# Performance work log

Measured on AMD Instinct MI355X. Metric: run time of the kernel, lower is better.

## Reference

```python
import jax, jax.numpy as jnp
import numpy as np

H_HEADS = 4
HEAD_QK = 64   # key_dim 256 / 4 heads
HEAD_V = 128   # value_dim 512 / 4 heads


def _ln(x, w, b, eps=1e-5):
    mu = jnp.mean(x, -1, keepdims=True)
    var = jnp.mean(jnp.square(x - mu), -1, keepdims=True)
    return (x - mu) / jnp.sqrt(var + eps) * w + b


def _gn(x, w, b, groups, eps=1e-5):
    # group norm over channel groups (per-head norm of WKV output)
    B, T, C = x.shape
    xg = x.reshape(B, T, groups, C // groups)
    mu = jnp.mean(xg, -1, keepdims=True)
    var = jnp.mean(jnp.square(xg - mu), -1, keepdims=True)
    xn = ((xg - mu) / jnp.sqrt(var + eps)).reshape(B, T, C)
    return xn * w + b


def _shift(x):
    # token shift: prepend zero, drop last (nn.ZeroPad2d((0,0,1,-1)))
    return jnp.pad(x, ((0, 0), (1, 0), (0, 0)))[:, :-1]


def setup_inputs() -> dict:
    key = jax.random.key(0)
    ks = jax.random.split(key, 32)
    B, T, C = 8, 4096, 512
    KD, VD = 256, 512        # key_dim = int(512*0.5), value_dim = int(512*1)
    LR, GLR = 32, 64         # proj_low_rank_dim, gate_low_rank_dim
    FF = 1024                # intermediate_size

    def nrm(k, shp, sc=0.02):
        return jax.random.normal(k, shp, dtype=jnp.float32) * sc

    return {
        "x": jax.random.normal(ks[0], (B, T, C), dtype=jnp.float32),
        "attn_ln_w": jnp.ones((C,), jnp.float32),
        "attn_ln_b": jnp.zeros((C,), jnp.float32),
        "mu_x": jax.random.uniform(ks[1], (C,), jnp.float32),
        "W_x1": nrm(ks[2], (C, 5 * LR)),
        "W_x2": nrm(ks[3], (5, LR, C)),
        "x_bias": jax.random.uniform(ks[4], (5, C), jnp.float32),
        "W_r": nrm(ks[5], (C, KD)),
        "W_k": nrm(ks[6], (C, KD)),
        "W_v": nrm(ks[7], (C, VD)),
        "W_g": nrm(ks[8], (C, VD)),
        "W_w1": nrm(ks[9], (C, GLR)),
        "W_w2": nrm(ks[10], (GLR, KD)),
        "b_w2": jax.random.uniform(ks[11], (KD,), jnp.float32, 0.5, 2.0),
        "u": nrm(ks[12], (H_HEADS, HEAD_QK), 0.5),
        "gn_w": jnp.ones((VD,), jnp.float32),
        "gn_b": jnp.zeros((VD,), jnp.float32),
        "W_o": nrm(ks[13], (VD, C)),
        "ffn_ln_w": jnp.ones((C,), jnp.float32),
        "ffn_ln_b": jnp.zeros((C,), jnp.float32),
        "mu_k": jax.random.uniform(ks[14], (C,), jnp.float32),
        "W_key": nrm(ks[15], (C, FF)),
        "mu_r": jax.random.uniform(ks[16], (C,), jnp.float32),
        "W_rec": nrm(ks[17], (C, C)),
        "W_val": nrm(ks[18], (FF, C)),
    }


def reference(x, attn_ln_w, attn_ln_b, mu_x, W_x1, W_x2, x_bias, W_r, W_k, W_v, W_g,
              W_w1, W_w2, b_w2, u, gn_w, gn_b, W_o, ffn_ln_w, ffn_ln_b,
              mu_k, W_key, mu_r, W_rec, W_val):
    B, T, C = x.shape
    H, K = H_HEADS, HEAD_QK

    # ---------- time mixing (RWKV6 attention) ----------
    res = x
    h = _ln(x, attn_ln_w, attn_ln_b)
    delta = _shift(h) - h
    # low-rank data-dependent lerp factors for (r, w, k, v, g)
    xx = jnp.tanh((h + delta * mu_x) @ W_x1).reshape(B, T, 5, -1)   # [B,T,5,LR]
    mus = jnp.einsum('btnr,nrh->btnh', xx, W_x2) + x_bias           # [B,T,5,C]
    mr, mw, mk, mv, mg = (mus[:, :, i] for i in range(5))
    r = ((h + delta * mr) @ W_r).reshape(B, T, H, K)
    w = jnp.tanh((h + delta * mw) @ W_w1) @ W_w2 + b_w2             # decay LoRA
    w = (-jnp.exp(w)).reshape(B, T, H, K)                           # log-decay <= 0
    k = ((h + delta * mk) @ W_k).reshape(B, T, H, K)
    v = ((h + delta * mv) @ W_v).reshape(B, T, H, -1)               # [B,T,H,V]
    g = (h + delta * mg) @ W_g                                      # output gate

    # WKV6 recurrence: o_t = r_t . (S + diag(u) k_t v_t^T); S <- diag(e^{w_t}) S + k_t v_t^T
    def step(S, inp):
        rt, kt, vt, wt = inp                      # [B,H,K],[B,H,K],[B,H,V],[B,H,K]
        kv = kt[..., :, None] * vt[..., None, :]  # [B,H,K,V]
        ot = jnp.einsum('bhk,bhkv->bhv', rt, S + u[None, :, :, None] * kv)
        return jnp.exp(wt)[..., None] * S + kv, ot

    S0 = jnp.zeros((B, H, K, v.shape[-1]), x.dtype)
    seq = (r.transpose(1, 0, 2, 3), k.transpose(1, 0, 2, 3),
           v.transpose(1, 0, 2, 3), w.transpose(1, 0, 2, 3))
    _, o = jax.lax.scan(step, S0, seq)            # o: [T,B,H,V]
    o = o.transpose(1, 0, 2, 3).reshape(B, T, -1)
    o = _gn(o, gn_w, gn_b, H) * jax.nn.silu(g)
    h = res + o @ W_o

    # ---------- channel mixing (RWKV6 FFN) ----------
    res = h
    hn = _ln(h, ffn_ln_w, ffn_ln_b)
    delta = _shift(hn) - hn
    kf = jnp.square(jax.nn.relu((hn + delta * mu_k) @ W_key))
    rf = jax.nn.sigmoid((hn + delta * mu_r) @ W_rec)
    return res + rf * (kf @ W_val)
```

## Files before the change

kernel.cpp:

```cpp
#include <hip/hip_runtime.h>
#include <hip/hip_bf16.h>
#include <hip/hip_fp16.h>
#include <math.h>

#define BB 8
#define TT 4096
#define CC 512
#define BT (BB*TT)
#define KD 256
#define VD 512
#define NSUB 64
#define SUB 64

using bf16 = __hip_bfloat16;
using f16 = _Float16;
typedef __attribute__((ext_vector_type(2))) float f32x2;
typedef __attribute__((ext_vector_type(4))) float f32x4;
typedef __attribute__((ext_vector_type(8))) short s16x8;
typedef __attribute__((ext_vector_type(8))) unsigned short u16x8;
typedef const __attribute__((address_space(1))) unsigned int gu32;
typedef __attribute__((address_space(3))) unsigned int lu32;

static __device__ __forceinline__ float bf2f(bf16 x){ return __bfloat162float(x); }
static __device__ __forceinline__ bf16 f2bf(float x){ return __float2bfloat16(x); }
static __device__ __forceinline__ float bfbits(unsigned short u){
  union { unsigned int i; float f; } x; x.i = ((unsigned int)u)<<16; return x.f;
}
static __device__ __forceinline__ unsigned short f2bfbits(float f){
  union { bf16 b; unsigned short u; } x; x.b = f2bf(f); return x.u;
}
static __device__ __forceinline__ float h2f(unsigned short u){
  f16 h; __builtin_memcpy(&h,&u,2); return (float)h;
}
static __device__ __forceinline__ void gload16(const void* g, void* l){
  __builtin_amdgcn_global_load_lds((gu32*)g, (lu32*)l, 16, 0, 0);
}

#define MiB 1048576ull
static constexpr size_t OFF_H1   = 0;
static constexpr size_t OFF_XX   = 32*MiB;
static constexpr size_t OFF_DSEG = 32*MiB;
static constexpr size_t OFF_HM   = 48*MiB;
static constexpr size_t OFF_R    = 80*MiB;
static constexpr size_t OFF_K    = 96*MiB;
static constexpr size_t OFF_V    = 112*MiB;
static constexpr size_t OFF_WD   = 144*MiB;
static constexpr size_t OFF_G    = 176*MiB;
static constexpr size_t OFF_W1T  = 208*MiB;
static constexpr size_t WT_X1  = 212*MiB;
static constexpr size_t WT_R   = WT_X1  + 262144;
static constexpr size_t WT_K   = WT_R   + 262144;
static constexpr size_t WT_V   = WT_K   + 262144;
static constexpr size_t WT_G   = WT_V   + 524288;
static constexpr size_t WT_W1  = WT_G   + 524288;
static constexpr size_t WT_W2  = WT_W1  + 65536;
static constexpr size_t WT_O   = WT_W2  + 32768;
static constexpr size_t WT_KEY = WT_O   + 524288;
static constexpr size_t WT_REC = WT_KEY + 1048576;
static constexpr size_t WT_VAL = WT_REC + 524288;
static constexpr size_t WT_X2T = WT_VAL + 1048576;
static constexpr size_t WS_NEED = WT_X2T + 163840;

__global__ __launch_bounds__(256) void wconv_t2(const float* s0, const float* s1, const float* s2,
        const float* s3, const float* s4, const float* s5, const float* s6, const float* s7,
        const float* s8, const float* s9, const float* s10, char* ws){
  struct E{int K,N,Npad; size_t off;};
  const E tab[11] = {
    {512,160,256,WT_X1},{512,256,256,WT_R},{512,256,256,WT_K},{512,512,512,WT_V},
    {512,512,512,WT_G},{512,64,64,WT_W1},{64,256,256,WT_W2},{512,512,512,WT_O},
    {512,1024,1024,WT_KEY},{512,512,512,WT_REC},{1024,512,512,WT_VAL}};
  const float* srcs[11] = {s0,s1,s2,s3,s4,s5,s6,s7,s8,s9,s10};
  int blk = blockIdx.x, i = 0, acc = 0;
  #pragma unroll 1
  for (; i<11; i++){ int nt = (tab[i].K>>6)*(tab[i].Npad>>6); if (blk < acc+nt) break; acc += nt; }
  int local = blk - acc;
  int K = tab[i].K, N = tab[i].N;
  int ntn = tab[i].Npad>>6;
  int k0 = (local/ntn)*64, n0 = (local%ntn)*64;
  const float* src = srcs[i];
  bf16* dst = (bf16*)(ws + tab[i].off);
  __shared__ float T[64][65];
  int t = threadIdx.x;
  #pragma unroll
  for (int e=0;e<16;e++){
    int idx = t + e*256; int r = idx>>6, c = idx&63;
    int n = n0 + c;
    T[r][c] = (n < N) ? src[(size_t)(k0+r)*N + n] : 0.f;
  }
  __syncthreads();
  #pragma unroll
  for (int e=0;e<16;e++){
    int idx = t + e*256; int r = idx>>6, c = idx&63;
    dst[(size_t)(n0+r)*K + k0 + c] = f2bf(T[c][r]);
  }
}

__global__ void wconv_x2(const float* __restrict__ src, bf16* __restrict__ dst){
  int idx = blockIdx.x*256 + threadIdx.x;
  int i = idx >> 14;
  int rem = idx & 16383;
  int c = rem >> 5, r = rem & 31;
  dst[idx] = f2bf(src[((size_t)i*32 + r)*512 + c]);
}

__global__ __launch_bounds__(256) void ln_bf16(const float* __restrict__ x, const float* __restrict__ w,
                                               const float* __restrict__ b, bf16* __restrict__ out){
  int bt = blockIdx.x;
  const float* row = x + (size_t)bt*CC;
  int t = threadIdx.x;
  float a0 = row[t], a1 = row[t+256];
  float s = a0 + a1, ss = a0*a0 + a1*a1;
  for (int off=32; off; off>>=1){ s += __shfl_down(s, off, 64); ss += __shfl_down(ss, off, 64); }
  __shared__ float ps[4], pss[4];
  int wv = t>>6, ln = t&63;
  if (ln==0){ ps[wv]=s; pss[wv]=ss; }
  __syncthreads();
  if (t==0){
    float S=ps[0]+ps[1]+ps[2]+ps[3], SS=pss[0]+pss[1]+pss[2]+pss[3];
    float mu = S/CC; float var = SS/CC - mu*mu;
    ps[0]=mu; pss[0]=rsqrtf(var+1e-5f);
  }
  __syncthreads();
  float mu = ps[0], inv = pss[0];
  out[(size_t)bt*CC + t]     = f2bf((a0-mu)*inv*w[t]+b[t]);
  out[(size_t)bt*CC + t+256] = f2bf((a1-mu)*inv*w[t+256]+b[t+256]);
}

__global__ void build_xm(const bf16* __restrict__ h, const float* __restrict__ mu_x, bf16* __restrict__ xm){
  size_t base = ((size_t)blockIdx.x*256 + threadIdx.x)*8;
  int c = (int)(base & (CC-1));
  size_t bt = base >> 9;
  u16x8 hv8 = *(const u16x8*)&((const unsigned short*)h)[base];
  u16x8 hp8;
  if (bt & (TT-1)) hp8 = *(const u16x8*)&((const unsigned short*)h)[base - CC];
  else { hp8 = u16x8{0,0,0,0,0,0,0,0}; }
  float m8[8];
  *(float4*)&m8[0] = *(const float4*)&mu_x[c];
  *(float4*)&m8[4] = *(const float4*)&mu_x[c+4];
  u16x8 o8;
  #pragma unroll
  for (int e=0;e<8;e++){
    float f = bfbits(hv8[e]), p = bfbits(hp8[e]);
    o8[e] = f2bfbits(f + (p-f)*m8[e]);
  }
  *(u16x8*)&((unsigned short*)xm)[base] = o8;
}

__global__ __launch_bounds__(256) void hm5_mfma(const bf16* __restrict__ h, const bf16* __restrict__ xx,
      const bf16* __restrict__ wx2t, const float* __restrict__ x_bias,
      bf16* __restrict__ hm0, bf16* __restrict__ hm1, bf16* __restrict__ hm2,
      bf16* __restrict__ hm3, bf16* __restrict__ hm4){
  __shared__ bf16 xxl[128][168];
  int bt0 = blockIdx.x*128;
  int c0 = blockIdx.y*128;
  int tid = threadIdx.x;
  #pragma unroll
  for (int p=0;p<10;p++){
    int idx = p*256 + tid;
    int row = idx/20, q = idx - row*20;
    *(uint4*)&xxl[row][q*8] = *(const uint4*)&xx[((size_t)(bt0+row))*256 + q*8];
  }
  __syncthreads();
  int wv = tid>>6, ln = tid&63;
  int wr = wv>>1, wc = wv&1;
  int ks = (ln>>4)*8;
  int l15 = ln&15;
  bf16* const outs[5] = {hm0,hm1,hm2,hm3,hm4};
  #pragma unroll
  for (int i=0;i<5;i++){
    s16x8 bq[4];
    #pragma unroll
    for (int ni=0;ni<4;ni++)
      bq[ni] = *(const s16x8*)&xxl[wc*64 + ni*16 + l15][i*32 + ks];
    f32x4 acc[4][4];
    #pragma unroll
    for (int mi=0;mi<4;mi++){
      int chb = c0 + wr*64 + mi*16 + (ln>>4)*4;
      float4 bia = *(const float4*)&x_bias[i*CC + chb];
      #pragma unroll
      for (int ni=0;ni<4;ni++){ f32x4 a = {bia.x,bia.y,bia.z,bia.w}; acc[mi][ni] = a; }
    }
    #pragma unroll
    for (int mi=0;mi<4;mi++){
      s16x8 aw = *(const s16x8*)&wx2t[((size_t)i*512 + c0 + wr*64 + mi*16 + l15)*32 + ks];
      #pragma unroll
      for (int ni=0;ni<4;ni++)
        acc[mi][ni] = __builtin_amdgcn_mfma_f32_16x16x32_bf16(aw, bq[ni], acc[mi][ni], 0,0,0);
    }
    bf16* o = outs[i];
    #pragma unroll
    for (int mi=0;mi<4;mi++){
      int ch = c0 + wr*64 + mi*16 + (ln>>4)*4;
      #pragma unroll
      for (int ni=0;ni<4;ni++){
        int tok = bt0 + wc*64 + ni*16 + l15;
        size_t base = (size_t)tok*CC + ch;
        ushort4 hv4 = *(const ushort4*)&((const unsigned short*)h)[base];
        ushort4 hp4;
        if (tok & (TT-1)) hp4 = *(const ushort4*)&((const unsigned short*)h)[base - CC];
        else { hp4.x=0; hp4.y=0; hp4.z=0; hp4.w=0; }
        ushort4 o4;
        float hv, hp, mus;
        hv = bfbits(hv4.x); hp = bfbits(hp4.x); mus = acc[mi][ni][0]; o4.x = f2bfbits(hv + (hp-hv)*mus);
        hv = bfbits(hv4.y); hp = bfbits(hp4.y); mus = acc[mi][ni][1]; o4.y = f2bfbits(hv + (hp-hv)*mus);
        hv = bfbits(hv4.z); hp = bfbits(hp4.z); mus = acc[mi][ni][2]; o4.z = f2bfbits(hv + (hp-hv)*mus);
        hv = bfbits(hv4.w); hp = bfbits(hp4.w); mus = acc[mi][ni][3]; o4.w = f2bfbits(hv + (hp-hv)*mus);
        *(ushort4*)&((unsigned short*)o)[base] = o4;
      }
    }
  }
}

enum {EP_BF16, EP_TANH_BF16, EP_NEGEXP_F16, EP_RES_F32, EP_RELU2_BF16, EP_SIG_BF16, EP_FINAL_F32};

template<int MODE>
__global__ __launch_bounds__(256) void gemm128(
    const bf16* __restrict__ A, const bf16* __restrict__ Bt, void* __restrict__ Out,
    int N, int K, const float* __restrict__ auxf, const bf16* __restrict__ auxb)
{
  __shared__ bf16 Al[128][32];
  __shared__ bf16 Bl[128][32];
  int tid = threadIdx.x;
  int nbk = N>>7;
  int q8 = gridDim.x>>3;
  int o = (blockIdx.x & 7)*q8 + (blockIdx.x>>3);
  int nb = o % nbk, mb = o / nbk;
  int m0 = mb*128, n0 = nb*128;
  int wv = tid>>6, ln = tid&63;
  int wr = wv>>1, wc = wv&1;
  f32x4 acc[4][4];
  #pragma unroll
  for (int i=0;i<4;i++) for (int j=0;j<4;j++){ f32x4 z={0.f,0.f,0.f,0.f}; acc[i][j]=z; }
  int r0 = tid>>2, k0 = (tid&3)*8;
  const int nkt = K>>5;
  for (int kt=0; kt<nkt; kt++){
    const bf16* ga = A  + (size_t)(m0+r0)*K + kt*32 + k0;
    const bf16* gb = Bt + (size_t)(n0+r0)*K + kt*32 + k0;
    gload16(ga,                 (char*)&Al[0][0] + tid*16);
    gload16(ga + (size_t)64*K,  (char*)&Al[0][0] + (tid+256)*16);
    gload16(gb,                 (char*)&Bl[0][0] + tid*16);
    gload16(gb + (size_t)64*K,  (char*)&Bl[0][0] + (tid+256)*16);
    __syncthreads();
    int ks = (ln>>4)*8;
    s16x8 af[4], bq[4];
    #pragma unroll
    for (int i=0;i<4;i++){
      af[i] = *(const s16x8*)&Al[wr*64 + i*16 + (ln&15)][ks];
      bq[i] = *(const s16x8*)&Bl[wc*64 + i*16 + (ln&15)][ks];
    }
    #pragma unroll
    for (int mi=0;mi<4;mi++)
      #pragma unroll
      for (int ni=0;ni<4;ni++)
        acc[mi][ni] = __builtin_amdgcn_mfma_f32_16x16x32_bf16(af[mi], bq[ni], acc[mi][ni], 0,0,0);
    __syncthreads();
  }
  #pragma unroll
  for (int mi=0;mi<4;mi++)
    #pragma unroll
    for (int ni=0;ni<4;ni++){
      int col = n0 + wc*64 + ni*16 + (ln&15);
      int rb  = m0 + wr*64 + mi*16 + (ln>>4)*4;
      #pragma unroll
      for (int j=0;j<4;j++){
        size_t idx = (size_t)(rb+j)*N + col;
        float val = acc[mi][ni][j];
        if constexpr(MODE==EP_BF16)           ((bf16*)Out)[idx] = f2bf(val);
        else if constexpr(MODE==EP_TANH_BF16) ((bf16*)Out)[idx] = f2bf(tanhf(val));
        else if constexpr(MODE==EP_RES_F32)   ((float*)Out)[idx] = auxf[idx] + val;
        else if constexpr(MODE==EP_RELU2_BF16){ float m = fmaxf(val,0.f); ((bf16*)Out)[idx] = f2bf(m*m); }
        else if constexpr(MODE==EP_SIG_BF16)  ((bf16*)Out)[idx] = f2bf(1.f/(1.f+expf(-val)));
        else if constexpr(MODE==EP_FINAL_F32) ((float*)Out)[idx] = auxf[idx] + bf2f(auxb[idx])*val;
      }
    }
}

template<int MODE>
__global__ __launch_bounds__(256) void gemm_bf16(
    const bf16* __restrict__ A, const bf16* __restrict__ Bt, void* __restrict__ Out,
    int N, int K, const float* __restrict__ bias)
{
  __shared__ bf16 Al[128][40];
  __shared__ bf16 Bl[64][40];
  int tid = threadIdx.x;
  int m0 = blockIdx.x*128, n0 = blockIdx.y*64;
  int wv = tid>>6, ln = tid&63;
  f32x4 acc[2][4];
  #pragma unroll
  for(int f=0;f<2;f++) for(int c=0;c<4;c++){ f32x4 z = {0.f,0.f,0.f,0.f}; acc[f][c]=z; }
  const int nkt = K>>5;
  for (int kt=0; kt<nkt; kt++){
    __syncthreads();
    {
      int c0 = tid, c1 = tid+256;
      int r = c0>>2, ko=(c0&3)*8;
      *(uint4*)&Al[r][ko] = *(const uint4*)&A[(size_t)(m0+r)*K + kt*32 + ko];
      r = c1>>2; ko=(c1&3)*8;
      *(uint4*)&Al[r][ko] = *(const uint4*)&A[(size_t)(m0+r)*K + kt*32 + ko];
      r = tid>>2; ko=(tid&3)*8;
      *(uint4*)&Bl[r][ko] = *(const uint4*)&Bt[(size_t)(n0+r)*K + kt*32 + ko];
    }
    __syncthreads();
    int ks = (ln>>4)*8;
    s16x8 af0 = *(const s16x8*)&Al[wv*32 + (ln&15)][ks];
    s16x8 af1 = *(const s16x8*)&Al[wv*32 + 16 + (ln&15)][ks];
    #pragma unroll
    for (int c=0;c<4;c++){
      s16x8 bfr = *(const s16x8*)&Bl[c*16 + (ln&15)][ks];
      acc[0][c] = __builtin_amdgcn_mfma_f32_16x16x32_bf16(af0, bfr, acc[0][c], 0,0,0);
      acc[1][c] = __builtin_amdgcn_mfma_f32_16x16x32_bf16(af1, bfr, acc[1][c], 0,0,0);
    }
  }
  #pragma unroll
  for (int f=0; f<2; f++) for (int c=0;c<4;c++){
    int col = n0 + c*16 + (ln&15);
    int rbase = m0 + wv*32 + f*16 + (ln>>4)*4;
    #pragma unroll
    for (int j=0;j<4;j++){
      size_t idx = (size_t)(rbase+j)*N + col;
      float val = acc[f][c][j];
      if constexpr(MODE==EP_TANH_BF16)      ((bf16*)Out)[idx] = f2bf(tanhf(val));
      else if constexpr(MODE==EP_NEGEXP_F16){
        float w = fmaxf(-expf(val + bias[col]), -20.f);
        ((f16*)Out)[idx] = (f16)expf(w);
      }
    }
  }
}

__global__ __launch_bounds__(128,3) void wkv_p1(const bf16* __restrict__ kbuf, const bf16* __restrict__ vbuf,
      const f16* __restrict__ ewb, bf16* __restrict__ Mseg, float* __restrict__ Dseg){
  int bhs = blockIdx.x; int bh = bhs>>6, sub = bhs&63;
  int b = bh>>2, h = bh&3;
  int tid = threadIdx.x, wv = tid>>6, ln = tid&63;
  __shared__ float vtile[16][132];
  int t0 = sub*SUB;
  size_t kqbase = ((size_t)b*TT + t0)*KD + h*64 + ln;
  float dacc = 1.f;
  f32x2 S2[32];
  #pragma unroll
  for (int p=0;p<32;p++){ f32x2 z={0.f,0.f}; S2[p]=z; }
  float wnxt = (float)ewb[kqbase];
  unsigned short qnxt = ((const unsigned short*)kbuf)[kqbase];
  #pragma unroll 1
  for (int tile=0; tile<4; tile++){
    int tb = t0 + tile*16;
    __syncthreads();
    {
      int t = tid>>3, c = (tid&7)*16;
      const unsigned short* vg = (const unsigned short*)vbuf + ((size_t)b*TT + tb + t)*VD + h*128 + c;
      u16x8 a8 = *(const u16x8*)vg;
      u16x8 b8 = *(const u16x8*)(vg+8);
      #pragma unroll
      for (int e=0;e<8;e++){ vtile[t][c+e] = bfbits(a8[e]); vtile[t][c+8+e] = bfbits(b8[e]); }
    }
    __syncthreads();
    #pragma unroll 1
    for (int tt=0;tt<16;tt++){
      int lt = tile*16+tt;
      float e = wnxt; unsigned short qcur = qnxt;
      if (lt < SUB-1){
        size_t gi = kqbase + (size_t)(lt+1)*KD;
        wnxt = (float)ewb[gi]; qnxt = ((const unsigned short*)kbuf)[gi];
      }
      dacc *= e;
      float qv = bfbits(qcur);
      f32x2 e2 = {e,e}, q2 = {qv,qv};
      #pragma unroll
      for (int vg=0;vg<16;vg++){
        f32x4 vvv = *(const f32x4*)&vtile[tt][wv*64 + vg*4];
        f32x2 vA = {vvv[0], vvv[1]}, vB = {vvv[2], vvv[3]};
        S2[vg*2]   = e2*S2[vg*2]   + q2*vA;
        S2[vg*2+1] = e2*S2[vg*2+1] + q2*vB;
      }
    }
  }
  unsigned short* M = (unsigned short*)Mseg + (size_t)bhs*8192 + (size_t)ln*128 + wv*64;
  #pragma unroll
  for (int vg=0; vg<16; vg++){
    ushort4 s4;
    s4.x = f2bfbits(S2[vg*2][0]);   s4.y = f2bfbits(S2[vg*2][1]);
    s4.z = f2bfbits(S2[vg*2+1][0]); s4.w = f2bfbits(S2[vg*2+1][1]);
    *(ushort4*)&M[vg*4] = s4;
  }
  if (wv==0) Dseg[(size_t)bhs*64 + ln] = dacc;
}

__global__ __launch_bounds__(256) void wkv_p2(bf16* __restrict__ MS, const float* __restrict__ Dseg){
  int idx = blockIdx.x*256 + threadIdx.x;
  int bh = idx>>13; int k = (idx>>7)&63; int v = idx&127;
  bf16* p = MS + (size_t)bh*NSUB*8192 + k*128 + v;
  const float* d = Dseg + (size_t)bh*NSUB*64 + k;
  float S = 0.f;
  float m = bf2f(p[0]); float D = d[0];
  #pragma unroll 1
  for (int seg=0; seg<NSUB; seg++){
    float mN=0.f, DN=0.f;
    if (seg < NSUB-1){ mN = bf2f(p[(size_t)(seg+1)*8192]); DN = d[(seg+1)*64]; }
    p[(size_t)seg*8192] = f2bf(S);
    S = D*S + m;
    m = mN; D = DN;
  }
}

__global__ __launch_bounds__(128,3) void wkv_p3(const bf16* __restrict__ rbuf, const bf16* __restrict__ kbuf,
     const bf16* __restrict__ vbuf, const f16* __restrict__ ewb, const bf16* __restrict__ Sstart,
     const float* __restrict__ uu, const bf16* __restrict__ gg,
     const float* __restrict__ gn_w, const float* __restrict__ gn_b, bf16* __restrict__ gated){
  int bhs = blockIdx.x; int bh = bhs>>6, sub = bhs&63;
  int b = bh>>2, h = bh&3;
  int tid = threadIdx.x;
  __shared__ float ew[8][68], qk[8][68], rr[8][68], bu[8];
  __shared__ unsigned short vtb[8][128];
  __shared__ float ot[8][132];
  int tq = tid>>4, cq4 = (tid&15)*4, cq8 = (tid&15)*8;
  float4 u4 = *(const float4*)&uu[h*64 + cq4];
  f32x2 S2[32];
  const unsigned short* Sst = (const unsigned short*)Sstart + (size_t)bhs*8192;
  #pragma unroll
  for (int p=0;p<32;p++){
    f32x2 s = { bfbits(Sst[(2*p)*128 + tid]), bfbits(Sst[(2*p+1)*128 + tid]) };
    S2[p] = s;
  }
  int t0 = sub*SUB;
  #pragma unroll 1
  for (int tile=0; tile<8; tile++){
    int tb = t0 + tile*8;
    {
      size_t gi = ((size_t)b*TT + tb + tq)*KD + h*64 + cq4;
      ushort4 e4s = *(const ushort4*)&((const unsigned short*)ewb)[gi];
      ew[tq][cq4+0]=h2f(e4s.x); ew[tq][cq4+1]=h2f(e4s.y); ew[tq][cq4+2]=h2f(e4s.z); ew[tq][cq4+3]=h2f(e4s.w);
      ushort4 k4 = *(const ushort4*)&((const unsigned short*)kbuf)[gi];
      ushort4 r4 = *(const ushort4*)&((const unsigned short*)rbuf)[gi];
      float q0=bfbits(k4.x),q1=bfbits(k4.y),q2=bfbits(k4.z),q3=bfbits(k4.w);
      float rv0=bfbits(r4.x),rv1=bfbits(r4.y),rv2=bfbits(r4.z),rv3=bfbits(r4.w);
      qk[tq][cq4+0]=q0; qk[tq][cq4+1]=q1; qk[tq][cq4+2]=q2; qk[tq][cq4+3]=q3;
      rr[tq][cq4+0]=rv0; rr[tq][cq4+1]=rv1; rr[tq][cq4+2]=rv2; rr[tq][cq4+3]=rv3;
      float part = rv0*q0*u4.x + rv1*q1*u4.y + rv2*q2*u4.z + rv3*q3*u4.w;
      part += __shfl_xor(part,1,64); part += __shfl_xor(part,2,64);
      part += __shfl_xor(part,4,64); part += __shfl_xor(part,8,64);
      if ((tid&15)==0) bu[tq] = part;
      *(u16x8*)&vtb[tq][cq8] = *(const u16x8*)&((const unsigned short*)vbuf)[((size_t)b*TT + tb + tq)*VD + h*128 + cq8];
    }
    __syncthreads();
    #pragma unroll 1
    for (int t=0;t<8;t++){
      float vl = bfbits(vtb[t][tid]);
      f32x2 vl2 = {vl, vl};
      f32x2 o2 = {0.f, 0.f};
      #pragma unroll
      for (int g=0;g<16;g++){
        f32x4 e4 = *(const f32x4*)&ew[t][g*4];
        f32x4 q4 = *(const f32x4*)&qk[t][g*4];
        f32x4 r4 = *(const f32x4*)&rr[t][g*4];
        f32x2 eA = {e4[0],e4[1]}, eB = {e4[2],e4[3]};
        f32x2 qA = {q4[0],q4[1]}, qB = {q4[2],q4[3]};
        f32x2 rA = {r4[0],r4[1]}, rB = {r4[2],r4[3]};
        int p = g*2;
        o2 += rA*S2[p];   S2[p]   = eA*S2[p]   + qA*vl2;
        o2 += rB*S2[p+1]; S2[p+1] = eB*S2[p+1] + qB*vl2;
      }
      float o = o2[0] + o2[1] + bu[t]*vl;
      ot[t][tid] = o;
    }
    __syncthreads();
    {
      float gw[8], gb[8];
      *(float4*)&gw[0] = *(const float4*)&gn_w[h*128+cq8];
      *(float4*)&gw[4] = *(const float4*)&gn_w[h*128+cq8+4];
      *(float4*)&gb[0] = *(const float4*)&gn_b[h*128+cq8];
      *(float4*)&gb[4] = *(const float4*)&gn_b[h*128+cq8+4];
      float o8[8];
      *(float4*)&o8[0] = *(const float4*)&ot[tq][cq8];
      *(float4*)&o8[4] = *(const float4*)&ot[tq][cq8+4];
      float s = 0.f, ss = 0.f;
      #pragma unroll
      for (int e=0;e<8;e++){ s += o8[e]; ss += o8[e]*o8[e]; }
      s += __shfl_xor(s,1,64); ss += __shfl_xor(ss,1,64);
      s += __shfl_xor(s,2,64); ss += __shfl_xor(ss,2,64);
      s += __shfl_xor(s,4,64); ss += __shfl_xor(ss,4,64);
      s += __shfl_xor(s,8,64); ss += __shfl_xor(ss,8,64);
      float mu = s*(1.f/128.f);
      float inv = rsqrtf(fmaxf(ss*(1.f/128.f) - mu*mu, 0.f) + 1e-5f);
      size_t go = ((size_t)b*TT + tb + tq)*VD + h*128 + cq8;
      u16x8 g8 = *(const u16x8*)&((const unsigned short*)gg)[go];
      u16x8 out8;
      #pragma unroll
      for (int e=0;e<8;e++){
        float xv = (o8[e]-mu)*inv*gw[e] + gb[e];
        float ga = bfbits(g8[e]);
        xv *= ga/(1.f+expf(-ga));
        out8[e] = f2bfbits(xv);
      }
      *(u16x8*)&((unsigned short*)gated)[go] = out8;
    }
    __syncthreads();
  }
}

__global__ void build_ffn_in(const bf16* __restrict__ hn, const float* __restrict__ mu_k,
                             const float* __restrict__ mu_r, bf16* __restrict__ kin, bf16* __restrict__ rin){
  size_t base = ((size_t)blockIdx.x*256 + threadIdx.x)*8;
  int c = (int)(base & (CC-1));
  size_t bt = base >> 9;
  u16x8 hv8 = *(const u16x8*)&((const unsigned short*)hn)[base];
  u16x8 hp8;
  if (bt & (TT-1)) hp8 = *(const u16x8*)&((const unsigned short*)hn)[base - CC];
  else { hp8 = u16x8{0,0,0,0,0,0,0,0}; }
  float mk8[8], mr8[8];
  *(float4*)&mk8[0] = *(const float4*)&mu_k[c];
  *(float4*)&mk8[4] = *(const float4*)&mu_k[c+4];
  *(float4*)&mr8[0] = *(const float4*)&mu_r[c];
  *(float4*)&mr8[4] = *(const float4*)&mu_r[c+4];
  u16x8 k8, r8;
  #pragma unroll
  for (int e=0;e<8;e++){
    float f = bfbits(hv8[e]), p = bfbits(hp8[e]);
    float d = p - f;
    k8[e] = f2bfbits(f + d*mk8[e]);
    r8[e] = f2bfbits(f + d*mr8[e]);
  }
  *(u16x8*)&((unsigned short*)kin)[base] = k8;
  *(u16x8*)&((unsigned short*)rin)[base] = r8;
}

extern "C" void kernel_launch(void* const* d_in, const int* in_sizes, int n_in,
                              void* d_out, int out_size, void* d_ws, size_t ws_size,
                              hipStream_t stream){
  (void)in_sizes; (void)n_in; (void)out_size;
  if (ws_size < WS_NEED) return;
  const float* x      = (const float*)d_in[0];
  const float* ln1w   = (const float*)d_in[1];
  const float* ln1b   = (const float*)d_in[2];
  const float* mu_x   = (const float*)d_in[3];
  const float* W_x1   = (const float*)d_in[4];
  const float* W_x2   = (const float*)d_in[5];
  const float* x_bias = (const float*)d_in[6];
  const float* W_r    = (const float*)d_in[7];
  const float* W_k    = (const float*)d_in[8];
  const float* W_v    = (const float*)d_in[9];
  const float* W_g    = (const float*)d_in[10];
  const float* W_w1   = (const float*)d_in[11];
  const float* W_w2   = (const float*)d_in[12];
  const float* b_w2   = (const float*)d_in[13];
  const float* u      = (const float*)d_in[14];
  const float* gn_w   = (const float*)d_in[15];
  const float* gn_b   = (const float*)d_in[16];
  const float* W_o    = (const float*)d_in[17];
  const float* ln2w   = (const float*)d_in[18];
  const float* ln2b   = (const float*)d_in[19];
  const float* mu_k   = (const float*)d_in[20];
  const float* W_key  = (const float*)d_in[21];
  const float* mu_r   = (const float*)d_in[22];
  const float* W_rec  = (const float*)d_in[23];
  const float* W_val  = (const float*)d_in[24];
  char* ws = (char*)d_ws;
  auto F  = [&](size_t off){ return (float*)(ws+off); };
  auto Bf = [&](size_t off){ return (bf16*)(ws+off); };
  float* h2 = (float*)d_out;
  bf16* Mseg = (bf16*)d_out;

  wconv_t2<<<620,256,0,stream>>>(W_x1,W_r,W_k,W_v,W_g,W_w1,W_w2,W_o,W_key,W_rec,W_val, ws);
  wconv_x2<<<320,256,0,stream>>>(W_x2, Bf(WT_X2T));

  ln_bf16<<<BT,256,0,stream>>>(x, ln1w, ln1b, Bf(OFF_H1));
  build_xm<<<BT*CC/8/256,256,0,stream>>>(Bf(OFF_H1), mu_x, Bf(OFF_HM));
  gemm128<EP_TANH_BF16><<<512,256,0,stream>>>(Bf(OFF_HM), Bf(WT_X1), Bf(OFF_XX), 256,512, nullptr,nullptr);

  bf16* hm1 = (bf16*)d_out;
  bf16* hm2 = (bf16*)((char*)d_out + 32*MiB);
  hm5_mfma<<<dim3(BT/128,4),256,0,stream>>>(Bf(OFF_H1), Bf(OFF_XX), Bf(WT_X2T), x_bias,
                                            Bf(OFF_HM), hm1, hm2, Bf(OFF_G), Bf(OFF_WD));
  gemm128<EP_BF16><<<512,256,0,stream>>>(Bf(OFF_HM), Bf(WT_R), Bf(OFF_R), 256,512, nullptr,nullptr);
  gemm_bf16<EP_TANH_BF16><<<dim3(BT/128,1),256,0,stream>>>(hm1, Bf(WT_W1), Bf(OFF_W1T), 64,512, nullptr);
  gemm128<EP_BF16><<<512,256,0,stream>>>(hm2, Bf(WT_K), Bf(OFF_K), 256,512, nullptr,nullptr);
  gemm128<EP_BF16><<<1024,256,0,stream>>>(Bf(OFF_G), Bf(WT_V), Bf(OFF_V), 512,512, nullptr,nullptr);
  gemm128<EP_BF16><<<1024,256,0,stream>>>(Bf(OFF_WD), Bf(WT_G), Bf(OFF_G), 512,512, nullptr,nullptr);
  gemm_bf16<EP_NEGEXP_F16><<<dim3(BT/128,4),256,0,stream>>>(Bf(OFF_W1T), Bf(WT_W2), (void*)F(OFF_WD), 256,64, b_w2);

  wkv_p1<<<BB*4*NSUB,128,0,stream>>>(Bf(OFF_K), Bf(OFF_V), (const f16*)F(OFF_WD), Mseg, F(OFF_DSEG));
  wkv_p2<<<BB*4*8192/256,256,0,stream>>>(Mseg, F(OFF_DSEG));
  wkv_p3<<<BB*4*NSUB,128,0,stream>>>(Bf(OFF_R), Bf(OFF_K), Bf(OFF_V), (const f16*)F(OFF_WD), Mseg, u,
                                     Bf(OFF_G), gn_w, gn_b, Bf(OFF_H1));

  gemm128<EP_RES_F32><<<1024,256,0,stream>>>(Bf(OFF_H1), Bf(WT_O), h2, 512,512, x,nullptr);

  ln_bf16<<<BT,256,0,stream>>>(h2, ln2w, ln2b, Bf(OFF_HM));
  build_ffn_in<<<BT*CC/8/256,256,0,stream>>>(Bf(OFF_HM), mu_k, mu_r, Bf(OFF_R), Bf(OFF_V));
  gemm128<EP_RELU2_BF16><<<2048,256,0,stream>>>(Bf(OFF_R), Bf(WT_KEY), Bf(OFF_WD), 1024,512, nullptr,nullptr);
  gemm128<EP_SIG_BF16><<<1024,256,0,stream>>>(Bf(OFF_V), Bf(WT_REC), Bf(OFF_H1), 512,512, nullptr,nullptr);
  gemm128<EP_FINAL_F32><<<1024,256,0,stream>>>(Bf(OFF_WD), Bf(WT_VAL), h2, 512,1024, h2, Bf(OFF_H1));
}
```

Baseline: 846.4 us.

## Batch independent projection GEMMs into grouped multi-GEMM launches

Adds a grouped GEMM kernel that takes a table of up to four independent GEMMs (K=512) and maps one flattened grid of 128x128 tiles across them, with an XCD-aware block remap. The four R/K/V/G projections and the two FFN key/receptance GEMMs now run as one launch each instead of separate launches. This cuts launch overhead and fills the tails between small GEMMs. The G output moves to a scratch buffer in d_out so it does not alias the WD input, and Mseg is relocated to compensate. The cost is a runtime mode branch in the epilogue and no double buffering in the shared load loop.

New measurement: 874.8 us. 1.03x slower.

```diff
diff --git a/kernel.cpp b/kernel.cpp
--- a/kernel.cpp
+++ b/kernel.cpp
@@ -271,6 +271,73 @@
         else if constexpr(MODE==EP_RELU2_BF16){ float m = fmaxf(val,0.f); ((bf16*)Out)[idx] = f2bf(m*m); }
         else if constexpr(MODE==EP_SIG_BF16)  ((bf16*)Out)[idx] = f2bf(1.f/(1.f+expf(-val)));
         else if constexpr(MODE==EP_FINAL_F32) ((float*)Out)[idx] = auxf[idx] + bf2f(auxb[idx])*val;
+      }
+    }
+}
+
+struct GEnt { const bf16* A; const bf16* Bt; bf16* Out; int N; int mode; int nblk; };
+struct GTab { GEnt e[4]; };
+
+__global__ __launch_bounds__(256) void gemm_multi(GTab tab, int total){
+  __shared__ bf16 Al[128][32];
+  __shared__ bf16 Bl[128][32];
+  int tid = threadIdx.x;
+  int q8 = total>>3;
+  int o = (blockIdx.x & 7)*q8 + (blockIdx.x>>3);
+  int i = 0, acc0 = 0;
+  #pragma unroll 1
+  for (; i<4; i++){ int nb = tab.e[i].nblk; if (o < acc0+nb) break; acc0 += nb; }
+  const bf16* A  = tab.e[i].A;
+  const bf16* Bt = tab.e[i].Bt;
+  bf16* Out = tab.e[i].Out;
+  int N = tab.e[i].N, mode = tab.e[i].mode;
+  int lo = o - acc0;
+  int nbk = N>>7;
+  int nb = lo % nbk, mb = lo / nbk;
+  int m0 = mb*128, n0 = nb*128;
+  int wv = tid>>6, ln = tid&63;
+  int wr = wv>>1, wc = wv&1;
+  f32x4 acc[4][4];
+  #pragma unroll
+  for (int a=0;a<4;a++) for (int b=0;b<4;b++){ f32x4 z={0.f,0.f,0.f,0.f}; acc[a][b]=z; }
+  int r0 = tid>>2, k0 = (tid&3)*8;
+  for (int kt=0; kt<16; kt++){
+    const bf16* ga = A  + (size_t)(m0+r0)*512 + kt*32 + k0;
+    const bf16* gb = Bt + (size_t)(n0+r0)*512 + kt*32 + k0;
+    gload16(ga,               (char*)&Al[0][0] + tid*16);
+    gload16(ga + (size_t)64*512, (char*)&Al[0][0] + (tid+256)*16);
+    gload16(gb,               (char*)&Bl[0][0] + tid*16);
+    gload16(gb + (size_t)64*512, (char*)&Bl[0][0] + (tid+256)*16);
+    __syncthreads();
+    int ks = (ln>>4)*8;
+    s16x8 af[4], bq[4];
+    #pragma unroll
+    for (int a=0;a<4;a++){
+      af[a] = *(const s16x8*)&Al[wr*64 + a*16 + (ln&15)][ks];
+      bq[a] = *(const s16x8*)&Bl[wc*64 + a*16 + (ln&15)][ks];
+    }
+    #pragma unroll
+    for (int mi=0;mi<4;mi++)
+      #pragma unroll
+      for (int ni=0;ni<4;ni++)
+        acc[mi][ni] = __builtin_amdgcn_mfma_f32_16x16x32_bf16(af[mi], bq[ni], acc[mi][ni], 0,0,0);
+    __syncthreads();
+  }
+  #pragma unroll
+  for (int mi=0;mi<4;mi++)
+    #pragma unroll
+    for (int ni=0;ni<4;ni++){
+      int col = n0 + wc*64 + ni*16 + (ln&15);
+      int rb  = m0 + wr*64 + mi*16 + (ln>>4)*4;
+      #pragma unroll
+      for (int j=0;j<4;j++){
+        size_t idx = (size_t)(rb+j)*N + col;
+        float val = acc[mi][ni][j];
+        float r;
+        if (mode == 0) r = val;
+        else if (mode == 1){ float m = fmaxf(val,0.f); r = m*m; }
+        else r = 1.f/(1.f+expf(-val));
+        Out[idx] = f2bf(r);
       }
     }
 }
@@ -558,7 +625,10 @@
   auto F  = [&](size_t off){ return (float*)(ws+off); };
   auto Bf = [&](size_t off){ return (bf16*)(ws+off); };
   float* h2 = (float*)d_out;
-  bf16* Mseg = (bf16*)d_out;
+  bf16* hm1 = (bf16*)d_out;
+  bf16* hm2 = (bf16*)((char*)d_out + 32*MiB);
+  bf16* gbuf = (bf16*)d_out;
+  bf16* Mseg = (bf16*)((char*)d_out + 32*MiB);
 
   wconv_t2<<<620,256,0,stream>>>(W_x1,W_r,W_k,W_v,W_g,W_w1,W_w2,W_o,W_key,W_rec,W_val, ws);
   wconv_x2<<<320,256,0,stream>>>(W_x2, Bf(WT_X2T));
@@ -567,27 +637,35 @@
   build_xm<<<BT*CC/8/256,256,0,stream>>>(Bf(OFF_H1), mu_x, Bf(OFF_HM));
   gemm128<EP_TANH_BF16><<<512,256,0,stream>>>(Bf(OFF_HM), Bf(WT_X1), Bf(OFF_XX), 256,512, nullptr,nullptr);
 
-  bf16* hm1 = (bf16*)d_out;
-  bf16* hm2 = (bf16*)((char*)d_out + 32*MiB);
   hm5_mfma<<<dim3(BT/128,4),256,0,stream>>>(Bf(OFF_H1), Bf(OFF_XX), Bf(WT_X2T), x_bias,
                                             Bf(OFF_HM), hm1, hm2, Bf(OFF_G), Bf(OFF_WD));
-  gemm128<EP_BF16><<<512,256,0,stream>>>(Bf(OFF_HM), Bf(WT_R), Bf(OFF_R), 256,512, nullptr,nullptr);
   gemm_bf16<EP_TANH_BF16><<<dim3(BT/128,1),256,0,stream>>>(hm1, Bf(WT_W1), Bf(OFF_W1T), 64,512, nullptr);
-  gemm128<EP_BF16><<<512,256,0,stream>>>(hm2, Bf(WT_K), Bf(OFF_K), 256,512, nullptr,nullptr);
-  gemm128<EP_BF16><<<1024,256,0,stream>>>(Bf(OFF_G), Bf(WT_V), Bf(OFF_V), 512,512, nullptr,nullptr);
-  gemm128<EP_BF16><<<1024,256,0,stream>>>(Bf(OFF_WD), Bf(WT_G), Bf(OFF_G), 512,512, nullptr,nullptr);
+  {
+    GTab t;
+    t.e[0] = {Bf(OFF_HM), Bf(WT_R), Bf(OFF_R), 256, 0, 512};
+    t.e[1] = {hm2,        Bf(WT_K), Bf(OFF_K), 256, 0, 512};
+    t.e[2] = {Bf(OFF_G),  Bf(WT_V), Bf(OFF_V), 512, 0, 1024};
+    t.e[3] = {Bf(OFF_WD), Bf(WT_G), gbuf,      512, 0, 1024};
+    gemm_multi<<<3072,256,0,stream>>>(t, 3072);
+  }
   gemm_bf16<EP_NEGEXP_F16><<<dim3(BT/128,4),256,0,stream>>>(Bf(OFF_W1T), Bf(WT_W2), (void*)F(OFF_WD), 256,64, b_w2);
 
   wkv_p1<<<BB*4*NSUB,128,0,stream>>>(Bf(OFF_K), Bf(OFF_V), (const f16*)F(OFF_WD), Mseg, F(OFF_DSEG));
   wkv_p2<<<BB*4*8192/256,256,0,stream>>>(Mseg, F(OFF_DSEG));
   wkv_p3<<<BB*4*NSUB,128,0,stream>>>(Bf(OFF_R), Bf(OFF_K), Bf(OFF_V), (const f16*)F(OFF_WD), Mseg, u,
-                                     Bf(OFF_G), gn_w, gn_b, Bf(OFF_H1));
+                                     gbuf, gn_w, gn_b, Bf(OFF_H1));
 
   gemm128<EP_RES_F32><<<1024,256,0,stream>>>(Bf(OFF_H1), Bf(WT_O), h2, 512,512, x,nullptr);
 
   ln_bf16<<<BT,256,0,stream>>>(h2, ln2w, ln2b, Bf(OFF_HM));
   build_ffn_in<<<BT*CC/8/256,256,0,stream>>>(Bf(OFF_HM), mu_k, mu_r, Bf(OFF_R), Bf(OFF_V));
-  gemm128<EP_RELU2_BF16><<<2048,256,0,stream>>>(Bf(OFF_R), Bf(WT_KEY), Bf(OFF_WD), 1024,512, nullptr,nullptr);
-  gemm128<EP_SIG_BF16><<<1024,256,0,stream>>>(Bf(OFF_V), Bf(WT_REC), Bf(OFF_H1), 512,512, nullptr,nullptr);
+  {
+    GTab t;
+    t.e[0] = {Bf(OFF_R), Bf(WT_KEY), Bf(OFF_WD), 1024, 1, 2048};
+    t.e[1] = {Bf(OFF_V), Bf(WT_REC), Bf(OFF_H1),  512, 2, 1024};
+    t.e[2] = {nullptr, nullptr, nullptr, 128, 0, 0};
+    t.e[3] = {nullptr, nullptr, nullptr, 128, 0, 0};
+    gemm_multi<<<3072,256,0,stream>>>(t, 3072);
+  }
   gemm128<EP_FINAL_F32><<<1024,256,0,stream>>>(Bf(OFF_WD), Bf(WT_VAL), h2, 512,1024, h2, Bf(OFF_H1));
 }
```

## Double WKV chunk kernels to 256 threads, splitting state across more lanes

Applied to the files above, without the earlier changes.

Both WKV chunk kernels (p1 state accumulation and p3 output pass) move from 128 to 256 threads per block. Each thread now holds half as much recurrent state, 32 floats instead of 64. In p1 the value dimension is split into quarters. In p3 the key dimension is split across two thread halves, whose partial outputs are summed through shared memory before the group norm. The aim is to raise occupancy and latency hiding on the sequential inner loop, at the cost of more shared-memory traffic, an extra reduction, and redundant per-thread loads of the shared decay and key scalars.

Measured after the change: 834.0 us. Within noise of the previous version (-1.5%).

```diff
diff --git a/kernel.cpp b/kernel.cpp
--- a/kernel.cpp
+++ b/kernel.cpp
@@ -328,18 +328,18 @@
   }
 }
 
-__global__ __launch_bounds__(128,3) void wkv_p1(const bf16* __restrict__ kbuf, const bf16* __restrict__ vbuf,
+__global__ __launch_bounds__(256) void wkv_p1(const bf16* __restrict__ kbuf, const bf16* __restrict__ vbuf,
       const f16* __restrict__ ewb, bf16* __restrict__ Mseg, float* __restrict__ Dseg){
   int bhs = blockIdx.x; int bh = bhs>>6, sub = bhs&63;
   int b = bh>>2, h = bh&3;
-  int tid = threadIdx.x, wv = tid>>6, ln = tid&63;
+  int tid = threadIdx.x, ln = tid&63, vq = tid>>6;
   __shared__ float vtile[16][132];
   int t0 = sub*SUB;
   size_t kqbase = ((size_t)b*TT + t0)*KD + h*64 + ln;
   float dacc = 1.f;
-  f32x2 S2[32];
-  #pragma unroll
-  for (int p=0;p<32;p++){ f32x2 z={0.f,0.f}; S2[p]=z; }
+  f32x2 S2[16];
+  #pragma unroll
+  for (int p=0;p<16;p++){ f32x2 z={0.f,0.f}; S2[p]=z; }
   float wnxt = (float)ewb[kqbase];
   unsigned short qnxt = ((const unsigned short*)kbuf)[kqbase];
   #pragma unroll 1
@@ -347,12 +347,13 @@
     int tb = t0 + tile*16;
     __syncthreads();
     {
-      int t = tid>>3, c = (tid&7)*16;
-      const unsigned short* vg = (const unsigned short*)vbuf + ((size_t)b*TT + tb + t)*VD + h*128 + c;
-      u16x8 a8 = *(const u16x8*)vg;
-      u16x8 b8 = *(const u16x8*)(vg+8);
-      #pragma unroll
-      for (int e=0;e<8;e++){ vtile[t][c+e] = bfbits(a8[e]); vtile[t][c+8+e] = bfbits(b8[e]); }
+      int t = tid>>4, c = (tid&15)*8;
+      u16x8 a8 = *(const u16x8*)&((const unsigned short*)vbuf)[((size_t)b*TT + tb + t)*VD + h*128 + c];
+      float4 lo, hi;
+      lo.x=bfbits(a8[0]); lo.y=bfbits(a8[1]); lo.z=bfbits(a8[2]); lo.w=bfbits(a8[3]);
+      hi.x=bfbits(a8[4]); hi.y=bfbits(a8[5]); hi.z=bfbits(a8[6]); hi.w=bfbits(a8[7]);
+      *(float4*)&vtile[t][c]   = lo;
+      *(float4*)&vtile[t][c+4] = hi;
     }
     __syncthreads();
     #pragma unroll 1
@@ -367,23 +368,23 @@
       float qv = bfbits(qcur);
       f32x2 e2 = {e,e}, q2 = {qv,qv};
       #pragma unroll
-      for (int vg=0;vg<16;vg++){
-        f32x4 vvv = *(const f32x4*)&vtile[tt][wv*64 + vg*4];
+      for (int vg=0;vg<8;vg++){
+        f32x4 vvv = *(const f32x4*)&vtile[tt][vq*32 + vg*4];
         f32x2 vA = {vvv[0], vvv[1]}, vB = {vvv[2], vvv[3]};
         S2[vg*2]   = e2*S2[vg*2]   + q2*vA;
         S2[vg*2+1] = e2*S2[vg*2+1] + q2*vB;
       }
     }
   }
-  unsigned short* M = (unsigned short*)Mseg + (size_t)bhs*8192 + (size_t)ln*128 + wv*64;
-  #pragma unroll
-  for (int vg=0; vg<16; vg++){
+  unsigned short* M = (unsigned short*)Mseg + (size_t)bhs*8192 + (size_t)ln*128 + vq*32;
+  #pragma unroll
+  for (int vg=0; vg<8; vg++){
     ushort4 s4;
     s4.x = f2bfbits(S2[vg*2][0]);   s4.y = f2bfbits(S2[vg*2][1]);
     s4.z = f2bfbits(S2[vg*2+1][0]); s4.w = f2bfbits(S2[vg*2+1][1]);
     *(ushort4*)&M[vg*4] = s4;
   }
-  if (wv==0) Dseg[(size_t)bhs*64 + ln] = dacc;
+  if (vq==0) Dseg[(size_t)bhs*64 + ln] = dacc;
 }
 
 __global__ __launch_bounds__(256) void wkv_p2(bf16* __restrict__ MS, const float* __restrict__ Dseg){
@@ -403,7 +404,7 @@
   }
 }
 
-__global__ __launch_bounds__(128,3) void wkv_p3(const bf16* __restrict__ rbuf, const bf16* __restrict__ kbuf,
+__global__ __launch_bounds__(256) void wkv_p3(const bf16* __restrict__ rbuf, const bf16* __restrict__ kbuf,
      const bf16* __restrict__ vbuf, const f16* __restrict__ ewb, const bf16* __restrict__ Sstart,
      const float* __restrict__ uu, const bf16* __restrict__ gg,
      const float* __restrict__ gn_w, const float* __restrict__ gn_b, bf16* __restrict__ gated){
@@ -412,14 +413,15 @@
   int tid = threadIdx.x;
   __shared__ float ew[8][68], qk[8][68], rr[8][68], bu[8];
   __shared__ unsigned short vtb[8][128];
-  __shared__ float ot[8][132];
-  int tq = tid>>4, cq4 = (tid&15)*4, cq8 = (tid&15)*8;
-  float4 u4 = *(const float4*)&uu[h*64 + cq4];
-  f32x2 S2[32];
+  __shared__ float otp[2][8][132];
+  int v = tid&127, kw = tid>>7, kbase = kw*32;
+  int tq = tid>>5, c2 = (tid&31)*2, cq4 = (tid&31)*4;
+  float2 u2 = *(const float2*)&uu[h*64 + c2];
+  f32x2 S2[16];
   const unsigned short* Sst = (const unsigned short*)Sstart + (size_t)bhs*8192;
   #pragma unroll
-  for (int p=0;p<32;p++){
-    f32x2 s = { bfbits(Sst[(2*p)*128 + tid]), bfbits(Sst[(2*p+1)*128 + tid]) };
+  for (int p=0;p<16;p++){
+    f32x2 s = { bfbits(Sst[(kbase+2*p)*128 + v]), bfbits(Sst[(kbase+2*p+1)*128 + v]) };
     S2[p] = s;
   }
   int t0 = sub*SUB;
@@ -427,32 +429,33 @@
   for (int tile=0; tile<8; tile++){
     int tb = t0 + tile*8;
     {
-      size_t gi = ((size_t)b*TT + tb + tq)*KD + h*64 + cq4;
-      ushort4 e4s = *(const ushort4*)&((const unsigned short*)ewb)[gi];
-      ew[tq][cq4+0]=h2f(e4s.x); ew[tq][cq4+1]=h2f(e4s.y); ew[tq][cq4+2]=h2f(e4s.z); ew[tq][cq4+3]=h2f(e4s.w);
-      ushort4 k4 = *(const ushort4*)&((const unsigned short*)kbuf)[gi];
-      ushort4 r4 = *(const ushort4*)&((const unsigned short*)rbuf)[gi];
-      float q0=bfbits(k4.x),q1=bfbits(k4.y),q2=bfbits(k4.z),q3=bfbits(k4.w);
-      float rv0=bfbits(r4.x),rv1=bfbits(r4.y),rv2=bfbits(r4.z),rv3=bfbits(r4.w);
-      qk[tq][cq4+0]=q0; qk[tq][cq4+1]=q1; qk[tq][cq4+2]=q2; qk[tq][cq4+3]=q3;
-      rr[tq][cq4+0]=rv0; rr[tq][cq4+1]=rv1; rr[tq][cq4+2]=rv2; rr[tq][cq4+3]=rv3;
-      float part = rv0*q0*u4.x + rv1*q1*u4.y + rv2*q2*u4.z + rv3*q3*u4.w;
+      size_t gi = ((size_t)b*TT + tb + tq)*KD + h*64 + c2;
+      ushort2 e2s = *(const ushort2*)&((const unsigned short*)ewb)[gi];
+      ew[tq][c2] = h2f(e2s.x); ew[tq][c2+1] = h2f(e2s.y);
+      ushort2 k2 = *(const ushort2*)&((const unsigned short*)kbuf)[gi];
+      ushort2 r2 = *(const ushort2*)&((const unsigned short*)rbuf)[gi];
+      float q0=bfbits(k2.x), q1=bfbits(k2.y);
+      float rv0=bfbits(r2.x), rv1=bfbits(r2.y);
+      qk[tq][c2]=q0; qk[tq][c2+1]=q1;
+      rr[tq][c2]=rv0; rr[tq][c2+1]=rv1;
+      float part = rv0*q0*u2.x + rv1*q1*u2.y;
       part += __shfl_xor(part,1,64); part += __shfl_xor(part,2,64);
       part += __shfl_xor(part,4,64); part += __shfl_xor(part,8,64);
-      if ((tid&15)==0) bu[tq] = part;
-      *(u16x8*)&vtb[tq][cq8] = *(const u16x8*)&((const unsigned short*)vbuf)[((size_t)b*TT + tb + tq)*VD + h*128 + cq8];
+      part += __shfl_xor(part,16,64);
+      if ((tid&31)==0) bu[tq] = part;
+      *(ushort4*)&vtb[tq][cq4] = *(const ushort4*)&((const unsigned short*)vbuf)[((size_t)b*TT + tb + tq)*VD + h*128 + cq4];
     }
     __syncthreads();
     #pragma unroll 1
     for (int t=0;t<8;t++){
-      float vl = bfbits(vtb[t][tid]);
+      float vl = bfbits(vtb[t][v]);
       f32x2 vl2 = {vl, vl};
       f32x2 o2 = {0.f, 0.f};
       #pragma unroll
-      for (int g=0;g<16;g++){
-        f32x4 e4 = *(const f32x4*)&ew[t][g*4];
-        f32x4 q4 = *(const f32x4*)&qk[t][g*4];
-        f32x4 r4 = *(const f32x4*)&rr[t][g*4];
+      for (int g=0;g<8;g++){
+        f32x4 e4 = *(const f32x4*)&ew[t][kbase + g*4];
+        f32x4 q4 = *(const f32x4*)&qk[t][kbase + g*4];
+        f32x4 r4 = *(const f32x4*)&rr[t][kbase + g*4];
         f32x2 eA = {e4[0],e4[1]}, eB = {e4[2],e4[3]};
         f32x2 qA = {q4[0],q4[1]}, qB = {q4[2],q4[3]};
         f32x2 rA = {r4[0],r4[1]}, rB = {r4[2],r4[3]};
@@ -460,39 +463,36 @@
         o2 += rA*S2[p];   S2[p]   = eA*S2[p]   + qA*vl2;
         o2 += rB*S2[p+1]; S2[p+1] = eB*S2[p+1] + qB*vl2;
       }
-      float o = o2[0] + o2[1] + bu[t]*vl;
-      ot[t][tid] = o;
+      float o = o2[0] + o2[1];
+      if (kw==0) o += bu[t]*vl;
+      otp[kw][t][v] = o;
     }
     __syncthreads();
     {
-      float gw[8], gb[8];
-      *(float4*)&gw[0] = *(const float4*)&gn_w[h*128+cq8];
-      *(float4*)&gw[4] = *(const float4*)&gn_w[h*128+cq8+4];
-      *(float4*)&gb[0] = *(const float4*)&gn_b[h*128+cq8];
-      *(float4*)&gb[4] = *(const float4*)&gn_b[h*128+cq8+4];
-      float o8[8];
-      *(float4*)&o8[0] = *(const float4*)&ot[tq][cq8];
-      *(float4*)&o8[4] = *(const float4*)&ot[tq][cq8+4];
+      float4 oA = *(const float4*)&otp[0][tq][cq4];
+      float4 oB = *(const float4*)&otp[1][tq][cq4];
+      float o4[4] = {oA.x+oB.x, oA.y+oB.y, oA.z+oB.z, oA.w+oB.w};
       float s = 0.f, ss = 0.f;
       #pragma unroll
-      for (int e=0;e<8;e++){ s += o8[e]; ss += o8[e]*o8[e]; }
+      for (int e=0;e<4;e++){ s += o4[e]; ss += o4[e]*o4[e]; }
       s += __shfl_xor(s,1,64); ss += __shfl_xor(ss,1,64);
       s += __shfl_xor(s,2,64); ss += __shfl_xor(ss,2,64);
       s += __shfl_xor(s,4,64); ss += __shfl_xor(ss,4,64);
       s += __shfl_xor(s,8,64); ss += __shfl_xor(ss,8,64);
+      s += __shfl_xor(s,16,64); ss += __shfl_xor(ss,16,64);
       float mu = s*(1.f/128.f);
       float inv = rsqrtf(fmaxf(ss*(1.f/128.f) - mu*mu, 0.f) + 1e-5f);
-      size_t go = ((size_t)b*TT + tb + tq)*VD + h*128 + cq8;
-      u16x8 g8 = *(const u16x8*)&((const unsigned short*)gg)[go];
-      u16x8 out8;
-      #pragma unroll
-      for (int e=0;e<8;e++){
-        float xv = (o8[e]-mu)*inv*gw[e] + gb[e];
-        float ga = bfbits(g8[e]);
-        xv *= ga/(1.f+expf(-ga));
-        out8[e] = f2bfbits(xv);
-      }
-      *(u16x8*)&((unsigned short*)gated)[go] = out8;
+      float4 gw4 = *(const float4*)&gn_w[h*128+cq4];
+      float4 gb4 = *(const float4*)&gn_b[h*128+cq4];
+      size_t go = ((size_t)b*TT + tb + tq)*VD + h*128 + cq4;
+      ushort4 g4 = *(const ushort4*)&((const unsigned short*)gg)[go];
+      ushort4 out4;
+      float xv, ga;
+      xv = (o4[0]-mu)*inv*gw4.x + gb4.x; ga = bfbits(g4.x); xv *= ga/(1.f+expf(-ga)); out4.x = f2bfbits(xv);
+      xv = (o4[1]-mu)*inv*gw4.y + gb4.y; ga = bfbits(g4.y); xv *= ga/(1.f+expf(-ga)); out4.y = f2bfbits(xv);
+      xv = (o4[2]-mu)*inv*gw4.z + gb4.z; ga = bfbits(g4.z); xv *= ga/(1.f+expf(-ga)); out4.z = f2bfbits(xv);
+      xv = (o4[3]-mu)*inv*gw4.w + gb4.w; ga = bfbits(g4.w); xv *= ga/(1.f+expf(-ga)); out4.w = f2bfbits(xv);
+      *(ushort4*)&((unsigned short*)gated)[go] = out4;
     }
     __syncthreads();
   }
@@ -578,9 +578,9 @@
   gemm128<EP_BF16><<<1024,256,0,stream>>>(Bf(OFF_WD), Bf(WT_G), Bf(OFF_G), 512,512, nullptr,nullptr);
   gemm_bf16<EP_NEGEXP_F16><<<dim3(BT/128,4),256,0,stream>>>(Bf(OFF_W1T), Bf(WT_W2), (void*)F(OFF_WD), 256,64, b_w2);
 
-  wkv_p1<<<BB*4*NSUB,128,0,stream>>>(Bf(OFF_K), Bf(OFF_V), (const f16*)F(OFF_WD), Mseg, F(OFF_DSEG));
+  wkv_p1<<<BB*4*NSUB,256,0,stream>>>(Bf(OFF_K), Bf(OFF_V), (const f16*)F(OFF_WD), Mseg, F(OFF_DSEG));
   wkv_p2<<<BB*4*8192/256,256,0,stream>>>(Mseg, F(OFF_DSEG));
-  wkv_p3<<<BB*4*NSUB,128,0,stream>>>(Bf(OFF_R), Bf(OFF_K), Bf(OFF_V), (const f16*)F(OFF_WD), Mseg, u,
+  wkv_p3<<<BB*4*NSUB,256,0,stream>>>(Bf(OFF_R), Bf(OFF_K), Bf(OFF_V), (const f16*)F(OFF_WD), Mseg, u,
                                      Bf(OFF_G), gn_w, gn_b, Bf(OFF_H1));
 
   gemm128<EP_RES_F32><<<1024,256,0,stream>>>(Bf(OFF_H1), Bf(WT_O), h2, 512,512, x,nullptr);
```
